# Optimization experiments

Measured on AMD Instinct MI355X. Metric: run time of the kernel, lower is better.

Reference implementation:

```python
import jax, jax.numpy as jnp
import numpy as np
from jax import lax

R = 512          # num RoIs
K = 81           # num classes (COCO + bg)
IM_H, IM_W = 800, 1333
WX, WY, WW, WH = 10.0, 10.0, 5.0, 5.0   # cfg.MODEL.BBOX_REG_WEIGHTS
XFORM_CLIP = float(np.log(1000.0 / 16.0))  # cfg.BBOX_XFORM_CLIP
NMS_THRESH = 0.5
SCORE_THRESH = 0.001
MAX_PER_IMG = 100
POST_NMS_TOPN = 300


def setup_inputs() -> dict:
    key = jax.random.key(0)
    k1, k2, k3, k4, k5, k6 = jax.random.split(key, 6)
    # Build valid RoIs inside the image (x1<x2, y1<y2)
    cx = jax.random.uniform(k1, (R,)) * IM_W
    cy = jax.random.uniform(k2, (R,)) * IM_H
    w = jax.random.uniform(k3, (R,)) * 200.0 + 20.0
    h = jax.random.uniform(k4, (R,)) * 200.0 + 20.0
    rois = jnp.stack([
        jnp.clip(cx - 0.5 * w, 0.0, IM_W - 1),
        jnp.clip(cy - 0.5 * h, 0.0, IM_H - 1),
        jnp.clip(cx + 0.5 * w, 0.0, IM_W - 1),
        jnp.clip(cy + 0.5 * h, 0.0, IM_H - 1),
    ], axis=1).astype(jnp.float32)
    deltas = (jax.random.normal(k5, (R, 4 * K)) * 0.3).astype(jnp.float32)
    scores = jax.nn.softmax(jax.random.normal(k6, (R, K)) * 2.0, axis=1).astype(jnp.float32)
    return {"rois": rois, "deltas": deltas, "scores": scores}


def bbox_transform(boxes, deltas):
    # boxes [R,4], deltas [R,4K] -> pred boxes [R,K,4], clamped to image
    widths = boxes[:, 2] - boxes[:, 0] + 1.0
    heights = boxes[:, 3] - boxes[:, 1] + 1.0
    ctr_x = boxes[:, 0] + 0.5 * widths
    ctr_y = boxes[:, 1] + 0.5 * heights
    d = deltas.reshape(-1, K, 4)  # [R,K,4]
    dx = d[:, :, 0] / WX
    dy = d[:, :, 1] / WY
    dw = jnp.minimum(d[:, :, 2] / WW, XFORM_CLIP)
    dh = jnp.minimum(d[:, :, 3] / WH, XFORM_CLIP)
    pcx = dx * widths[:, None] + ctr_x[:, None]
    pcy = dy * heights[:, None] + ctr_y[:, None]
    pw = jnp.exp(dw) * widths[:, None]
    ph = jnp.exp(dh) * heights[:, None]
    x1 = jnp.clip(pcx - 0.5 * pw, 0.0, IM_W - 1)
    y1 = jnp.clip(pcy - 0.5 * ph, 0.0, IM_H - 1)
    x2 = jnp.clip(pcx + 0.5 * pw - 1.0, 0.0, IM_W - 1)
    y2 = jnp.clip(pcy + 0.5 * ph - 1.0, 0.0, IM_H - 1)
    return jnp.stack([x1, y1, x2, y2], axis=-1)  # [R,K,4]


def nms_one_class(scores_c, boxes_c):
    # Greedy NMS for one class. scores_c [R], boxes_c [R,4] -> keep mask [R] (orig order)
    order = jnp.argsort(-scores_c)
    b = boxes_c[order]
    areas = (b[:, 2] - b[:, 0] + 1.0) * (b[:, 3] - b[:, 1] + 1.0)
    xx1 = jnp.maximum(b[:, None, 0], b[None, :, 0])
    yy1 = jnp.maximum(b[:, None, 1], b[None, :, 1])
    xx2 = jnp.minimum(b[:, None, 2], b[None, :, 2])
    yy2 = jnp.minimum(b[:, None, 3], b[None, :, 3])
    inter = jnp.maximum(xx2 - xx1 + 1.0, 0.0) * jnp.maximum(yy2 - yy1 + 1.0, 0.0)
    iou = inter / (areas[:, None] + areas[None, :] - inter)
    suppress = iou > NMS_THRESH  # [R,R]
    idx = jnp.arange(R)

    def body(i, keep):
        sup = suppress[i] & keep[i] & (idx > i)
        return keep & (~sup)

    keep = lax.fori_loop(0, R, body, jnp.ones((R,), bool))
    keep = keep & (jnp.cumsum(keep) <= POST_NMS_TOPN)
    return jnp.zeros((R,), bool).at[order].set(keep)


def _detect(rois, deltas, scores):
    boxes3 = bbox_transform(rois, deltas)  # [R,K,4]
    # valid classes: max score over rois (excluding bg) above threshold
    cls_valid = jnp.concatenate([
        jnp.zeros((1,), bool),
        scores[:, 1:].max(axis=0) > SCORE_THRESH,
    ])  # [K]
    keep_kc = jax.vmap(nms_one_class, in_axes=(1, 1))(scores, boxes3)  # [K,R]
    nms_mask = (keep_kc.T & cls_valid[None, :]).astype(scores.dtype)  # [R,K]
    dists_all = nms_mask * scores
    # duplicate filtering: one label per box
    scores_pre = dists_all.max(axis=1)   # [R]
    labels_pre = dists_all.argmax(axis=1)
    order = jnp.argsort(-scores_pre)
    top = order[:MAX_PER_IMG]            # [100]
    scores_all = scores_pre[top]
    labels_all = labels_pre[top]
    valid = scores_all > SCORE_THRESH
    boxes_assign = boxes3.reshape(-1, 4)[top * K + labels_all]  # [100,4]
    scores_all = jnp.where(valid, scores_all, 0.0)
    boxes_assign = jnp.where(valid[:, None], boxes_assign, 0.0)
    out = jnp.concatenate([scores_all[:, None], boxes_assign], axis=1)  # [100,5]
    return out, labels_all, top


def reference(rois, deltas, scores):
    return _detect(rois, deltas, scores)
```

## Files before the change

kernel.cpp:

```cpp
#include <hip/hip_runtime.h>
#include <cstdint>
#include <cstddef>


#define R 512
#define K 81
#define IM_W_MAX 1332.0f
#define IM_H_MAX 799.0f
#define XFORM_CLIP_F 4.135166556742356f
#define NMS_THRESH_F 0.5f
#define SCORE_THRESH_F 0.001f
#define MAX_PER_IMG 100
#define POST_NMS_TOPN 300

__device__ __forceinline__ float4 transform_box(const float* __restrict__ rois,
                                                const float* __restrict__ deltas,
                                                int r, int k) {
    float4 roi = ((const float4*)rois)[r];
    float4 d4  = *(const float4*)(deltas + (size_t)r * (4 * K) + 4 * k);
    float w  = roi.z - roi.x + 1.0f;
    float h  = roi.w - roi.y + 1.0f;
    float cx = roi.x + 0.5f * w;
    float cy = roi.y + 0.5f * h;
    float dx = d4.x / 10.0f;
    float dy = d4.y / 10.0f;
    float dw = fminf(d4.z / 5.0f, XFORM_CLIP_F);
    float dh = fminf(d4.w / 5.0f, XFORM_CLIP_F);
    float pcx = dx * w + cx;
    float pcy = dy * h + cy;
    float pw  = expf(dw) * w;
    float ph  = expf(dh) * h;
    float4 b;
    b.x = fminf(fmaxf(pcx - 0.5f * pw, 0.0f), IM_W_MAX);
    b.y = fminf(fmaxf(pcy - 0.5f * ph, 0.0f), IM_H_MAX);
    b.z = fminf(fmaxf(pcx + 0.5f * pw - 1.0f, 0.0f), IM_W_MAX);
    b.w = fminf(fmaxf(pcy + 0.5f * ph - 1.0f, 0.0f), IM_H_MAX);
    return b;
}

__global__ void __launch_bounds__(512)
rank_boxes_kernel(const float* __restrict__ rois,
                  const float* __restrict__ deltas,
                  const float* __restrict__ scores,
                  float4* __restrict__ sbox_g,
                  int* __restrict__ order_g,
                  float* __restrict__ ssc_g,
                  int* __restrict__ valid_g) {
    const int k = blockIdx.x, tid = threadIdx.x;
    __shared__ unsigned long long s_key[R];
    __shared__ float s_red[R];

    const float sc = scores[tid * K + k];
    {
        unsigned int bits = __float_as_uint(sc);
        s_key[tid] = ((unsigned long long)(~bits) << 32) | (unsigned int)tid;
    }
    s_red[tid] = sc;
    __syncthreads();
    for (int s = 256; s > 0; s >>= 1) {
        if (tid < s) s_red[tid] = fmaxf(s_red[tid], s_red[tid + s]);
        __syncthreads();
    }
    const bool valid = (k != 0) && (s_red[0] > SCORE_THRESH_F);
    if (tid == 0) valid_g[k] = valid;
    if (!valid) return;

    const unsigned long long ki = s_key[tid];
    int cnt = 0;
    const ulonglong2* kp = (const ulonglong2*)s_key;
    #pragma unroll 8
    for (int j2 = 0; j2 < R / 2; ++j2) {
        ulonglong2 k2 = kp[j2];
        cnt += (k2.x < ki);
        cnt += (k2.y < ki);
    }
    sbox_g[k * R + cnt]  = transform_box(rois, deltas, tid, k);
    order_g[k * R + cnt] = tid;
    ssc_g[k * R + cnt]   = sc;
}

__global__ void __launch_bounds__(256)
bitmatrix_kernel(const float4* __restrict__ sbox_g,
                 const int* __restrict__ valid_g,
                 unsigned long long* __restrict__ supT_g) {
    const int b = blockIdx.x;
    const int k = b >> 3;
    const int w = b & 7;
    const int tid = threadIdx.x;
    if (!valid_g[k]) return;

    __shared__ float4 s_sbox[R];
    __shared__ float  s_area[R];
    for (int i = tid; i < R; i += 256) {
        float4 bx = sbox_g[k * R + i];
        s_sbox[i] = bx;
        s_area[i] = (bx.z - bx.x + 1.0f) * (bx.w - bx.y + 1.0f);
    }
    __syncthreads();

    const int jbase = w * 64;
    #pragma unroll
    for (int rep = 0; rep < 2; ++rep) {
        const int i = tid + rep * 256;
        const int d = i - jbase;
        unsigned long long mask =
            (d < 0) ? ~0ull : ((d >= 63) ? 0ull : (~0ull << (d + 1)));
        unsigned long long bits = 0ull;
        if (mask) {
            const float4 bi = s_sbox[i];
            const float  ai = s_area[i];
            #pragma unroll 8
            for (int jj = 0; jj < 64; ++jj) {
                float4 bj = s_sbox[jbase + jj];
                float  aj = s_area[jbase + jj];
                float xx1 = fmaxf(bi.x, bj.x);
                float yy1 = fmaxf(bi.y, bj.y);
                float xx2 = fminf(bi.z, bj.z);
                float yy2 = fminf(bi.w, bj.w);
                float iw = fmaxf(xx2 - xx1 + 1.0f, 0.0f);
                float ih = fmaxf(yy2 - yy1 + 1.0f, 0.0f);
                float inter = iw * ih;
                float denom = ai + aj - inter;
                float two_i = inter + inter;
                float hi = denom * 1.0000002f;
                float lo = denom * 0.99999976f;
                bool sup = two_i > hi;
                if (!sup && !(two_i < lo)) {
                    sup = (inter / denom) > NMS_THRESH_F;
                }
                bits |= (unsigned long long)sup << jj;
            }
        }
        supT_g[k * 4096 + w * 512 + i] = bits & mask;
    }
}

__global__ void __launch_bounds__(64)
sweep_kernel(const unsigned long long* __restrict__ supT_g,
             const int* __restrict__ order_g,
             const float* __restrict__ ssc_g,
             const int* __restrict__ valid_g,
             float* __restrict__ dists_t) {
    const int k = blockIdx.x;
    const int l = threadIdx.x;

    if (!valid_g[k]) {
        #pragma unroll
        for (int p = 0; p < 8; ++p) dists_t[k * R + p * 64 + l] = 0.0f;
        return;
    }

    int   ord[8];
    float ssc[8];
    #pragma unroll
    for (int p = 0; p < 8; ++p) {
        ord[p] = order_g[k * R + p * 64 + l];
        ssc[p] = ssc_g[k * R + p * 64 + l];
    }

    const unsigned long long* base = supT_g + (size_t)k * 4096;
    unsigned long long rrow[8], rnext[8];
    #pragma unroll
    for (int w = 0; w < 8; ++w) rrow[w] = base[w * 512 + l];

    unsigned long long kb[8];
    #pragma unroll
    for (int w = 0; w < 8; ++w) kb[w] = ~0ull;

    #pragma unroll
    for (int wb = 0; wb < 8; ++wb) {
        if (wb < 7) {
            #pragma unroll
            for (int w = 0; w < 8; ++w)
                rnext[w] = (w > wb) ? base[w * 512 + (wb + 1) * 64 + l] : 0ull;
        }

        const unsigned long long nz = __ballot(rrow[wb] != 0ull);
        unsigned long long cur = kb[wb];
        unsigned long long m = cur & nz;
        while (m) {
            int bit = __builtin_ctzll(m);
            const unsigned int r_lo = (unsigned int)(rrow[wb] & 0xffffffffull);
            const unsigned int r_hi = (unsigned int)(rrow[wb] >> 32);
            unsigned long long row =
                ((unsigned long long)(unsigned int)__builtin_amdgcn_readlane((int)r_hi, bit) << 32) |
                 (unsigned long long)(unsigned int)__builtin_amdgcn_readlane((int)r_lo, bit);
            m &= m - 1;
            cur &= ~row;
            m   &= ~row;
        }
        kb[wb] = cur;

        #pragma unroll
        for (int w = wb + 1; w < 8; ++w) {
            unsigned long long contrib = ((cur >> l) & 1ull) ? rrow[w] : 0ull;
            if (__ballot(contrib != 0ull)) {
                #pragma unroll
                for (int off = 32; off > 0; off >>= 1)
                    contrib |= __shfl_xor(contrib, off, 64);
                kb[w] &= ~contrib;
            }
        }

        #pragma unroll
        for (int w = 0; w < 8; ++w) rrow[w] = rnext[w];
    }

    int total = 0;
    #pragma unroll
    for (int w = 0; w < 8; ++w) total += __popcll(kb[w]);
    if (total > POST_NMS_TOPN) {
        int cnt = 0;
        #pragma unroll
        for (int w = 0; w < 8; ++w) {
            int pc = __popcll(kb[w]);
            if (cnt + pc <= POST_NMS_TOPN) { cnt += pc; continue; }
            unsigned long long word = kb[w], outw = 0ull;
            int room = POST_NMS_TOPN - cnt;
            while (room > 0) {
                unsigned long long lsb = word & (~word + 1ull);
                outw |= lsb; word ^= lsb; --room;
            }
            kb[w] = outw; cnt = POST_NMS_TOPN;
        }
    }

    #pragma unroll
    for (int p = 0; p < 8; ++p)
        dists_t[k * R + ord[p]] = ((kb[p] >> l) & 1ull) ? ssc[p] : 0.0f;
}

__global__ void __launch_bounds__(512)
finalize_kernel(const float* __restrict__ dists_t,
                const float* __restrict__ rois,
                const float* __restrict__ deltas,
                float* __restrict__ out) {
    const int b = blockIdx.x;
    const int t = threadIdx.x;
    __shared__ unsigned long long s_key[R];
    __shared__ int s_arg[R];

    {
        const int r = t;
        float vmax = dists_t[r];
        int arg = 0;
        #pragma unroll 8
        for (int kk = 1; kk < K; ++kk) {
            float v = dists_t[kk * R + r];
            if (v > vmax) { vmax = v; arg = kk; }
        }
        unsigned int bits = __float_as_uint(vmax);
        s_key[r] = ((unsigned long long)(~bits) << 32) | (unsigned int)r;
        s_arg[r] = arg;
    }
    __syncthreads();

    const int ri = b * 64 + (t >> 3);
    const int c  = t & 7;
    const unsigned long long ki = s_key[ri];
    int cnt = 0;
    #pragma unroll 8
    for (int j = 0; j < 64; ++j) {
        int jj = (j + c * 8) & 63;
        cnt += (s_key[c * 64 + jj] < ki);
    }
    cnt += __shfl_xor(cnt, 1, 64);
    cnt += __shfl_xor(cnt, 2, 64);
    cnt += __shfl_xor(cnt, 4, 64);

    if (c == 0 && cnt < MAX_PER_IMG) {
        float vmax = __uint_as_float(~(unsigned int)(ki >> 32));
        int arg = s_arg[ri];
        bool valid = vmax > SCORE_THRESH_F;
        float4 bx = transform_box(rois, deltas, ri, arg);
        out[cnt * 5 + 0] = valid ? vmax : 0.0f;
        out[cnt * 5 + 1] = valid ? bx.x : 0.0f;
        out[cnt * 5 + 2] = valid ? bx.y : 0.0f;
        out[cnt * 5 + 3] = valid ? bx.z : 0.0f;
        out[cnt * 5 + 4] = valid ? bx.w : 0.0f;
        out[500 + cnt] = (float)arg;
        out[600 + cnt] = (float)ri;
    }
}

extern "C" void kernel_launch(void* const* d_in, const int* in_sizes, int n_in,
                              void* d_out, int out_size, void* d_ws, size_t ws_size,
                              hipStream_t stream) {
    const float* rois   = (const float*)d_in[0];
    const float* deltas = (const float*)d_in[1];
    const float* scores = (const float*)d_in[2];
    float* out = (float*)d_out;

    char* ws = (char*)d_ws;
    float4* sbox_g  = (float4*)(ws + 0);
    int*    order_g = (int*)   (ws + 663552);
    float*  ssc_g   = (float*) (ws + 829440);
    int*    valid_g = (int*)   (ws + 995328);
    float*  dists_t = (float*) (ws + 995840);
    unsigned long long* supT_g = (unsigned long long*)(ws + 1161728);

    rank_boxes_kernel<<<K, 512, 0, stream>>>(rois, deltas, scores,
                                             sbox_g, order_g, ssc_g, valid_g);
    bitmatrix_kernel <<<K * 8, 256, 0, stream>>>(sbox_g, valid_g, supT_g);
    sweep_kernel     <<<K, 64, 0, stream>>>(supT_g, order_g, ssc_g, valid_g, dists_t);
    finalize_kernel  <<<8, 512, 0, stream>>>(dists_t, rois, deltas, out);
}
```

Measured before the change: 108.4 us.

## Fuse rank, IoU bitmatrix and NMS sweep into one per-class kernel

Merges the three per-class kernels (ranking/box transform, IoU suppression bitmatrix, greedy sweep) into a single 512-thread block per class that keeps the sorted boxes and the suppression matrix in shared memory. The bitmatrix work is also packed into a triangular index space so only the needed word entries are computed, with no idle threads on empty entries. This removes two kernel launches and the global round-trips of sorted boxes, order, scores and the bit matrix. The cost is less parallelism in the IoU phase (81 blocks instead of 648) and heavy shared memory use (~56KB), which limits occupancy.

```diff
diff --git a/kernel.cpp b/kernel.cpp
--- a/kernel.cpp
+++ b/kernel.cpp
@@ -38,17 +38,38 @@
     return b;
 }
 
+__device__ __forceinline__ bool iou_sup(float4 bi, float ai, float4 bj, float aj) {
+    float xx1 = fmaxf(bi.x, bj.x);
+    float yy1 = fmaxf(bi.y, bj.y);
+    float xx2 = fminf(bi.z, bj.z);
+    float yy2 = fminf(bi.w, bj.w);
+    float iw = fmaxf(xx2 - xx1 + 1.0f, 0.0f);
+    float ih = fmaxf(yy2 - yy1 + 1.0f, 0.0f);
+    float inter = iw * ih;
+    float denom = ai + aj - inter;
+    float two_i = inter + inter;
+    bool sup = two_i > denom * 1.0000002f;
+    if (!sup && !(two_i < denom * 0.99999976f)) {
+        sup = (inter / denom) > NMS_THRESH_F;
+    }
+    return sup;
+}
+
 __global__ void __launch_bounds__(512)
-rank_boxes_kernel(const float* __restrict__ rois,
-                  const float* __restrict__ deltas,
-                  const float* __restrict__ scores,
-                  float4* __restrict__ sbox_g,
-                  int* __restrict__ order_g,
-                  float* __restrict__ ssc_g,
-                  int* __restrict__ valid_g) {
+detect_class_kernel(const float* __restrict__ rois,
+                    const float* __restrict__ deltas,
+                    const float* __restrict__ scores,
+                    float* __restrict__ dists_t) {
     const int k = blockIdx.x, tid = threadIdx.x;
+
+    __shared__ unsigned long long s_supT[4096];
+    __shared__ float4 s_sbox[R];
+    __shared__ float  s_area[R];
     __shared__ unsigned long long s_key[R];
-    __shared__ float s_red[R];
+    __shared__ float  s_red[R];
+    __shared__ float  s_ssc[R];
+    __shared__ int    s_ord[R];
+    __shared__ unsigned long long s_keep[8];
 
     const float sc = scores[tid * K + k];
     {
@@ -56,178 +77,128 @@
         s_key[tid] = ((unsigned long long)(~bits) << 32) | (unsigned int)tid;
     }
     s_red[tid] = sc;
+    #pragma unroll
+    for (int j = 0; j < 8; ++j) s_supT[tid + (j << 9)] = 0ull;
     __syncthreads();
     for (int s = 256; s > 0; s >>= 1) {
         if (tid < s) s_red[tid] = fmaxf(s_red[tid], s_red[tid + s]);
         __syncthreads();
     }
     const bool valid = (k != 0) && (s_red[0] > SCORE_THRESH_F);
-    if (tid == 0) valid_g[k] = valid;
-    if (!valid) return;
-
-    const unsigned long long ki = s_key[tid];
-    int cnt = 0;
-    const ulonglong2* kp = (const ulonglong2*)s_key;
-    #pragma unroll 8
-    for (int j2 = 0; j2 < R / 2; ++j2) {
-        ulonglong2 k2 = kp[j2];
-        cnt += (k2.x < ki);
-        cnt += (k2.y < ki);
-    }
-    sbox_g[k * R + cnt]  = transform_box(rois, deltas, tid, k);
-    order_g[k * R + cnt] = tid;
-    ssc_g[k * R + cnt]   = sc;
-}
-
-__global__ void __launch_bounds__(256)
-bitmatrix_kernel(const float4* __restrict__ sbox_g,
-                 const int* __restrict__ valid_g,
-                 unsigned long long* __restrict__ supT_g) {
-    const int b = blockIdx.x;
-    const int k = b >> 3;
-    const int w = b & 7;
-    const int tid = threadIdx.x;
-    if (!valid_g[k]) return;
-
-    __shared__ float4 s_sbox[R];
-    __shared__ float  s_area[R];
-    for (int i = tid; i < R; i += 256) {
-        float4 bx = sbox_g[k * R + i];
-        s_sbox[i] = bx;
-        s_area[i] = (bx.z - bx.x + 1.0f) * (bx.w - bx.y + 1.0f);
-    }
-    __syncthreads();
-
-    const int jbase = w * 64;
-    #pragma unroll
-    for (int rep = 0; rep < 2; ++rep) {
-        const int i = tid + rep * 256;
+    if (!valid) {
+        dists_t[k * R + tid] = 0.0f;
+        return;
+    }
+
+    {
+        const unsigned long long ki = s_key[tid];
+        int cnt = 0;
+        const ulonglong2* kp = (const ulonglong2*)s_key;
+        #pragma unroll 8
+        for (int j2 = 0; j2 < R / 2; ++j2) {
+            ulonglong2 k2 = kp[j2];
+            cnt += (k2.x < ki);
+            cnt += (k2.y < ki);
+        }
+        float4 b = transform_box(rois, deltas, tid, k);
+        s_sbox[cnt] = b;
+        s_area[cnt] = (b.z - b.x + 1.0f) * (b.w - b.y + 1.0f);
+        s_ord[cnt]  = tid;
+        s_ssc[cnt]  = sc;
+    }
+    __syncthreads();
+
+    for (int u = tid; u < 2296; u += 512) {
+        int w8 = (u >= 63) + (u >= 190) + (u >= 381) + (u >= 636) +
+                 (u >= 955) + (u >= 1338) + (u >= 1785);
+        int i = u - w8 * (32 * w8 + 31);
+        const int jbase = w8 << 6;
+        const float4 bi = s_sbox[i];
+        const float  ai = s_area[i];
         const int d = i - jbase;
-        unsigned long long mask =
-            (d < 0) ? ~0ull : ((d >= 63) ? 0ull : (~0ull << (d + 1)));
+        unsigned long long mask = (d < 0) ? ~0ull : (~0ull << (d + 1));
         unsigned long long bits = 0ull;
-        if (mask) {
-            const float4 bi = s_sbox[i];
-            const float  ai = s_area[i];
-            #pragma unroll 8
-            for (int jj = 0; jj < 64; ++jj) {
-                float4 bj = s_sbox[jbase + jj];
-                float  aj = s_area[jbase + jj];
-                float xx1 = fmaxf(bi.x, bj.x);
-                float yy1 = fmaxf(bi.y, bj.y);
-                float xx2 = fminf(bi.z, bj.z);
-                float yy2 = fminf(bi.w, bj.w);
-                float iw = fmaxf(xx2 - xx1 + 1.0f, 0.0f);
-                float ih = fmaxf(yy2 - yy1 + 1.0f, 0.0f);
-                float inter = iw * ih;
-                float denom = ai + aj - inter;
-                float two_i = inter + inter;
-                float hi = denom * 1.0000002f;
-                float lo = denom * 0.99999976f;
-                bool sup = two_i > hi;
-                if (!sup && !(two_i < lo)) {
-                    sup = (inter / denom) > NMS_THRESH_F;
-                }
-                bits |= (unsigned long long)sup << jj;
-            }
-        }
-        supT_g[k * 4096 + w * 512 + i] = bits & mask;
-    }
-}
-
-__global__ void __launch_bounds__(64)
-sweep_kernel(const unsigned long long* __restrict__ supT_g,
-             const int* __restrict__ order_g,
-             const float* __restrict__ ssc_g,
-             const int* __restrict__ valid_g,
-             float* __restrict__ dists_t) {
-    const int k = blockIdx.x;
-    const int l = threadIdx.x;
-
-    if (!valid_g[k]) {
+        #pragma unroll 8
+        for (int jj = 0; jj < 64; ++jj) {
+            float4 bj = s_sbox[jbase + jj];
+            float  aj = s_area[jbase + jj];
+            bits |= (unsigned long long)iou_sup(bi, ai, bj, aj) << jj;
+        }
+        s_supT[(w8 << 9) + i] = bits & mask;
+    }
+    __syncthreads();
+
+    if (tid < 64) {
+        const int l = tid;
+        unsigned long long kb[8];
         #pragma unroll
-        for (int p = 0; p < 8; ++p) dists_t[k * R + p * 64 + l] = 0.0f;
-        return;
-    }
-
-    int   ord[8];
-    float ssc[8];
-    #pragma unroll
-    for (int p = 0; p < 8; ++p) {
-        ord[p] = order_g[k * R + p * 64 + l];
-        ssc[p] = ssc_g[k * R + p * 64 + l];
-    }
-
-    const unsigned long long* base = supT_g + (size_t)k * 4096;
-    unsigned long long rrow[8], rnext[8];
-    #pragma unroll
-    for (int w = 0; w < 8; ++w) rrow[w] = base[w * 512 + l];
-
-    unsigned long long kb[8];
-    #pragma unroll
-    for (int w = 0; w < 8; ++w) kb[w] = ~0ull;
-
-    #pragma unroll
-    for (int wb = 0; wb < 8; ++wb) {
-        if (wb < 7) {
+        for (int w = 0; w < 8; ++w) kb[w] = ~0ull;
+        unsigned long long rrow[8];
+
+        #pragma unroll
+        for (int wb = 0; wb < 8; ++wb) {
             #pragma unroll
             for (int w = 0; w < 8; ++w)
-                rnext[w] = (w > wb) ? base[w * 512 + (wb + 1) * 64 + l] : 0ull;
-        }
-
-        const unsigned long long nz = __ballot(rrow[wb] != 0ull);
-        unsigned long long cur = kb[wb];
-        unsigned long long m = cur & nz;
-        while (m) {
-            int bit = __builtin_ctzll(m);
-            const unsigned int r_lo = (unsigned int)(rrow[wb] & 0xffffffffull);
-            const unsigned int r_hi = (unsigned int)(rrow[wb] >> 32);
-            unsigned long long row =
-                ((unsigned long long)(unsigned int)__builtin_amdgcn_readlane((int)r_hi, bit) << 32) |
-                 (unsigned long long)(unsigned int)__builtin_amdgcn_readlane((int)r_lo, bit);
-            m &= m - 1;
-            cur &= ~row;
-            m   &= ~row;
-        }
-        kb[wb] = cur;
-
+                if (w >= wb) rrow[w] = s_supT[(w << 9) + (wb << 6) + l];
+
+            const unsigned long long nz = __ballot(rrow[wb] != 0ull);
+            unsigned long long cur = kb[wb];
+            unsigned long long m = cur & nz;
+            while (m) {
+                int bit = __builtin_ctzll(m);
+                const unsigned int r_lo = (unsigned int)(rrow[wb] & 0xffffffffull);
+                const unsigned int r_hi = (unsigned int)(rrow[wb] >> 32);
+                unsigned long long row =
+                    ((unsigned long long)(unsigned int)__builtin_amdgcn_readlane((int)r_hi, bit) << 32) |
+                     (unsigned long long)(unsigned int)__builtin_amdgcn_readlane((int)r_lo, bit);
+                m &= m - 1;
+                cur &= ~row;
+                m   &= ~row;
+            }
+            kb[wb] = cur;
+
+            #pragma unroll
+            for (int w = wb + 1; w < 8; ++w) {
+                unsigned long long contrib = ((cur >> l) & 1ull) ? rrow[w] : 0ull;
+                if (__ballot(contrib != 0ull)) {
+                    #pragma unroll
+                    for (int off = 32; off > 0; off >>= 1)
+                        contrib |= __shfl_xor(contrib, off, 64);
+                    kb[w] &= ~contrib;
+                }
+            }
+        }
+
+        int total = 0;
         #pragma unroll
-        for (int w = wb + 1; w < 8; ++w) {
-            unsigned long long contrib = ((cur >> l) & 1ull) ? rrow[w] : 0ull;
-            if (__ballot(contrib != 0ull)) {
-                #pragma unroll
-                for (int off = 32; off > 0; off >>= 1)
-                    contrib |= __shfl_xor(contrib, off, 64);
-                kb[w] &= ~contrib;
+        for (int w = 0; w < 8; ++w) total += __popcll(kb[w]);
+        if (total > POST_NMS_TOPN) {
+            int cnt = 0;
+            #pragma unroll
+            for (int w = 0; w < 8; ++w) {
+                int pc = __popcll(kb[w]);
+                if (cnt + pc <= POST_NMS_TOPN) { cnt += pc; continue; }
+                unsigned long long word = kb[w], outw = 0ull;
+                int room = POST_NMS_TOPN - cnt;
+                while (room > 0) {
+                    unsigned long long lsb = word & (~word + 1ull);
+                    outw |= lsb; word ^= lsb; --room;
+                }
+                kb[w] = outw; cnt = POST_NMS_TOPN;
             }
         }
 
-        #pragma unroll
-        for (int w = 0; w < 8; ++w) rrow[w] = rnext[w];
-    }
-
-    int total = 0;
-    #pragma unroll
-    for (int w = 0; w < 8; ++w) total += __popcll(kb[w]);
-    if (total > POST_NMS_TOPN) {
-        int cnt = 0;
-        #pragma unroll
-        for (int w = 0; w < 8; ++w) {
-            int pc = __popcll(kb[w]);
-            if (cnt + pc <= POST_NMS_TOPN) { cnt += pc; continue; }
-            unsigned long long word = kb[w], outw = 0ull;
-            int room = POST_NMS_TOPN - cnt;
-            while (room > 0) {
-                unsigned long long lsb = word & (~word + 1ull);
-                outw |= lsb; word ^= lsb; --room;
-            }
-            kb[w] = outw; cnt = POST_NMS_TOPN;
-        }
-    }
-
-    #pragma unroll
-    for (int p = 0; p < 8; ++p)
-        dists_t[k * R + ord[p]] = ((kb[p] >> l) & 1ull) ? ssc[p] : 0.0f;
+        if (l == 0) {
+            s_keep[0] = kb[0]; s_keep[1] = kb[1];
+            s_keep[2] = kb[2]; s_keep[3] = kb[3];
+            s_keep[4] = kb[4]; s_keep[5] = kb[5];
+            s_keep[6] = kb[6]; s_keep[7] = kb[7];
+        }
+    }
+    __syncthreads();
+
+    const bool kept = (s_keep[tid >> 6] >> (tid & 63)) & 1ull;
+    dists_t[k * R + s_ord[tid]] = kept ? s_ssc[tid] : 0.0f;
 }
 
 __global__ void __launch_bounds__(512)
@@ -291,17 +262,8 @@
     const float* scores = (const float*)d_in[2];
     float* out = (float*)d_out;
 
-    char* ws = (char*)d_ws;
-    float4* sbox_g  = (float4*)(ws + 0);
-    int*    order_g = (int*)   (ws + 663552);
-    float*  ssc_g   = (float*) (ws + 829440);
-    int*    valid_g = (int*)   (ws + 995328);
-    float*  dists_t = (float*) (ws + 995840);
-    unsigned long long* supT_g = (unsigned long long*)(ws + 1161728);
-
-    rank_boxes_kernel<<<K, 512, 0, stream>>>(rois, deltas, scores,
-                                             sbox_g, order_g, ssc_g, valid_g);
-    bitmatrix_kernel <<<K * 8, 256, 0, stream>>>(sbox_g, valid_g, supT_g);
-    sweep_kernel     <<<K, 64, 0, stream>>>(supT_g, order_g, ssc_g, valid_g, dists_t);
-    finalize_kernel  <<<8, 512, 0, stream>>>(dists_t, rois, deltas, out);
-}
+    float* dists_t = (float*)d_ws;
+
+    detect_class_kernel<<<K, 512, 0, stream>>>(rois, deltas, scores, dists_t);
+    finalize_kernel    <<<8, 512, 0, stream>>>(dists_t, rois, deltas, out);
+}
```

Result: slower. 119.9 us (+10.6%).
